# Performance work log

Measured on AMD Instinct MI355X. Metric: run time of the kernel, lower is better.

## Reference

```python
import jax, jax.numpy as jnp
import numpy as np

H = 1024      # hidden_size
V = 50257     # output_size (vocab)
L = 10        # max_length

def setup_inputs() -> dict:
    key = jax.random.key(0)
    ks = jax.random.split(key, 16)
    s = 0.02
    f = jnp.float32
    return {
        "input_idx": jax.random.randint(ks[0], (1,), 0, V),
        "hidden": jax.random.normal(ks[1], (1, 1, H), f),
        "encoder_output": jax.random.normal(ks[2], (1, H), f),      # unused by forward (as in source)
        "encoder_outputs": jax.random.normal(ks[3], (L, H), f),
        "emb": jax.random.normal(ks[4], (V, H), f) * s,
        "attn_W": jax.random.normal(ks[5], (L, 2 * H), f) * s,
        "attn_b": jnp.zeros((L,), f),
        "comb_W": jax.random.normal(ks[6], (H, 2 * H), f) * s,
        "comb_b": jnp.zeros((H,), f),
        "W_ih": jax.random.normal(ks[7], (3 * H, H), f) * s,
        "W_hh": jax.random.normal(ks[8], (3 * H, H), f) * s,
        "b_ih": jnp.zeros((3 * H,), f),
        "b_hh": jnp.zeros((3 * H,), f),
        "out_W": jax.random.normal(ks[9], (V, H), f) * s,
        "out_b": jnp.zeros((V,), f),
    }

def reference(input_idx, hidden, encoder_output, encoder_outputs,
              emb, attn_W, attn_b, comb_W, comb_b,
              W_ih, W_hh, b_ih, b_hh, out_W, out_b):
    # embedding lookup, dropout = identity (eval mode)
    embedded = emb[input_idx]                       # [1, H]
    h0 = hidden[0]                                  # [1, H]
    # additive attention over encoder outputs
    concat = jnp.concatenate([embedded, h0], axis=1)            # [1, 2H]
    attn_weights = jax.nn.softmax(concat @ attn_W.T + attn_b, axis=1)  # [1, L]
    attn_applied = attn_weights @ encoder_outputs               # [1, H]
    # combine + relu
    x = jnp.concatenate([embedded, attn_applied], axis=1) @ comb_W.T + comb_b  # [1, H]
    x = jax.nn.relu(x)
    # single GRU step (torch gate order: r, z, n)
    gi = x @ W_ih.T + b_ih                          # [1, 3H]
    gh = h0 @ W_hh.T + b_hh                         # [1, 3H]
    ir, iz, in_ = jnp.split(gi, 3, axis=1)
    hr, hz, hn = jnp.split(gh, 3, axis=1)
    r = jax.nn.sigmoid(ir + hr)
    z = jax.nn.sigmoid(iz + hz)
    n = jnp.tanh(in_ + r * hn)
    h_new = (1.0 - z) * n + z * h0                  # [1, H]
    # output projection + log-softmax
    output = jax.nn.log_softmax(h_new @ out_W.T + out_b, axis=1)  # [1, V]
    return output, h_new[None], attn_weights
```

## Files before the change

kernel.cpp:

```cpp
#include <hip/hip_runtime.h>
#include <hip/hip_bf16.h>
#include <math.h>

#define H 1024
#define V 50257
#define L 10

#define OUT_ROWS_PER_BLOCK 16
#define OUT_NBLOCKS ((V + OUT_ROWS_PER_BLOCK - 1) / OUT_ROWS_PER_BLOCK)

#define WS_CONCAT   0
#define WS_X        2048
#define WS_GH       3072
#define WS_HNEW     6144
#define WS_LOGITS   8192
#define WS_PAIRS    58880

__device__ __forceinline__ float wave_reduce(float acc) {
    #pragma unroll
    for (int off = 32; off > 0; off >>= 1) acc += __shfl_down(acc, off);
    return acc;
}

__global__ void k_attn(const int* __restrict__ idx,
                       const float* __restrict__ hidden,
                       const float* __restrict__ enc_outs,
                       const float* __restrict__ emb,
                       const float* __restrict__ attn_W,
                       const float* __restrict__ attn_b,
                       float* __restrict__ ws,
                       float* __restrict__ attnw_out) {
    __shared__ float s_w[16];
    const int t = threadIdx.x;
    const int wave = t >> 6, lane = t & 63;
    const float* erow = emb + (size_t)idx[0] * H;

    for (int i = t; i < H; i += 640) ws[WS_CONCAT + i] = erow[i];

    if (wave < L) {
        const float4* w4 = (const float4*)(attn_W + (size_t)wave * 2 * H);
        const float4* e4 = (const float4*)erow;
        const float4* h4 = (const float4*)hidden;
        float acc = 0.f;
        #pragma unroll
        for (int i = lane; i < 512; i += 64) {
            float4 a = w4[i];
            float4 x = (i < 256) ? e4[i] : h4[i - 256];
            acc += a.x * x.x + a.y * x.y + a.z * x.z + a.w * x.w;
        }
        acc = wave_reduce(acc);
        if (lane == 0) s_w[wave] = acc + attn_b[wave];
    }
    __syncthreads();
    if (t == 0) {
        float m = -1e30f;
        #pragma unroll
        for (int l = 0; l < L; ++l) m = fmaxf(m, s_w[l]);
        float s = 0.f;
        #pragma unroll
        for (int l = 0; l < L; ++l) { s_w[l] = expf(s_w[l] - m); s += s_w[l]; }
        float inv = 1.f / s;
        #pragma unroll
        for (int l = 0; l < L; ++l) s_w[l] *= inv;
    }
    __syncthreads();
    if (t < L) attnw_out[t] = s_w[t];

    for (int i = t; i < H; i += 640) {
        float acc = 0.f;
        #pragma unroll
        for (int l = 0; l < L; ++l) acc += s_w[l] * enc_outs[l * H + i];
        ws[WS_CONCAT + H + i] = acc;
    }
}

__global__ void k_comb_gh(const float* __restrict__ comb_W,
                          const float* __restrict__ comb_b,
                          const float* __restrict__ W_hh,
                          const float* __restrict__ b_hh,
                          const float* __restrict__ hidden,
                          float* __restrict__ ws) {
    const int wave = threadIdx.x >> 6, lane = threadIdx.x & 63;
    if (blockIdx.x < 256) {
        const int row = blockIdx.x * 4 + wave;
        const float4* w4 = (const float4*)(comb_W + (size_t)row * 2 * H);
        const float4* v4 = (const float4*)(ws + WS_CONCAT);
        float acc = 0.f;
        #pragma unroll
        for (int i = lane; i < 512; i += 64) {
            float4 a = w4[i], x = v4[i];
            acc += a.x * x.x + a.y * x.y + a.z * x.z + a.w * x.w;
        }
        acc = wave_reduce(acc);
        if (lane == 0) ws[WS_X + row] = fmaxf(acc + comb_b[row], 0.f);
    } else {
        const int row = (blockIdx.x - 256) * 4 + wave;
        const float4* w4 = (const float4*)(W_hh + (size_t)row * H);
        const float4* v4 = (const float4*)hidden;
        float acc = 0.f;
        #pragma unroll
        for (int i = lane; i < 256; i += 64) {
            float4 a = w4[i], x = v4[i];
            acc += a.x * x.x + a.y * x.y + a.z * x.z + a.w * x.w;
        }
        acc = wave_reduce(acc);
        if (lane == 0) ws[WS_GH + row] = acc + b_hh[row];
    }
}

__global__ void k_gi_gru(const float* __restrict__ W_ih,
                         const float* __restrict__ b_ih,
                         const float* __restrict__ hidden,
                         float* __restrict__ ws,
                         float* __restrict__ h_out) {
    const int wave = threadIdx.x >> 6, lane = threadIdx.x & 63;
    const int j = blockIdx.x * 16 + wave;
    const float4* xv = (const float4*)(ws + WS_X);
    const float4* w0 = (const float4*)(W_ih + (size_t)j * H);
    const float4* w1 = (const float4*)(W_ih + (size_t)(H + j) * H);
    const float4* w2 = (const float4*)(W_ih + (size_t)(2 * H + j) * H);
    float a0 = 0.f, a1 = 0.f, a2 = 0.f;
    #pragma unroll
    for (int i = lane; i < 256; i += 64) {
        float4 x = xv[i];
        float4 b;
        b = w0[i]; a0 += b.x * x.x + b.y * x.y + b.z * x.z + b.w * x.w;
        b = w1[i]; a1 += b.x * x.x + b.y * x.y + b.z * x.z + b.w * x.w;
        b = w2[i]; a2 += b.x * x.x + b.y * x.y + b.z * x.z + b.w * x.w;
    }
    a0 = wave_reduce(a0);
    a1 = wave_reduce(a1);
    a2 = wave_reduce(a2);
    if (lane == 0) {
        const float ir = a0 + b_ih[j];
        const float iz = a1 + b_ih[H + j];
        const float in_ = a2 + b_ih[2 * H + j];
        const float hr = ws[WS_GH + j];
        const float hz = ws[WS_GH + H + j];
        const float hn = ws[WS_GH + 2 * H + j];
        const float r = 1.f / (1.f + expf(-(ir + hr)));
        const float z = 1.f / (1.f + expf(-(iz + hz)));
        const float n = tanhf(in_ + r * hn);
        const float h0j = hidden[j];
        const float h = (1.f - z) * n + z * h0j;
        ws[WS_HNEW + j] = h;
        h_out[j] = h;
    }
}

__global__ void k_out_mv(const float* __restrict__ out_W,
                         const float* __restrict__ out_b,
                         const float* __restrict__ ws_in,
                         float* __restrict__ logits,
                         float* __restrict__ pairs) {
    __shared__ float sm[4], ss[4];
    const int wave = threadIdx.x >> 6, lane = threadIdx.x & 63;
    const int base = blockIdx.x * OUT_ROWS_PER_BLOCK + wave * 4;
    const float4* v4 = (const float4*)(ws_in + WS_HNEW);
    float vals[4];
    int nvalid = 0;
    #pragma unroll
    for (int k = 0; k < 4; ++k) {
        const int row = base + k;
        if (row >= V) break;
        const float4* w4 = (const float4*)(out_W + (size_t)row * H);
        float acc = 0.f;
        #pragma unroll
        for (int i = lane; i < 256; i += 64) {
            float4 a = w4[i], x = v4[i];
            acc += a.x * x.x + a.y * x.y + a.z * x.z + a.w * x.w;
        }
        acc = wave_reduce(acc);
        if (lane == 0) {
            const float val = acc + out_b[row];
            logits[row] = val;
            vals[nvalid] = val;
        }
        ++nvalid;
    }
    if (lane == 0) {
        float m = -INFINITY, s = 0.f;
        for (int k = 0; k < nvalid; ++k) m = fmaxf(m, vals[k]);
        for (int k = 0; k < nvalid; ++k) s += expf(vals[k] - m);
        sm[wave] = m; ss[wave] = s;
    }
    __syncthreads();
    if (threadIdx.x == 0) {
        float m = -INFINITY, s = 0.f;
        #pragma unroll
        for (int w = 0; w < 4; ++w) {
            const float pm = sm[w], psv = ss[w];
            if (pm == -INFINITY) continue;
            if (m == -INFINITY) { m = pm; s = psv; }
            else if (pm <= m)   { s += psv * expf(pm - m); }
            else                { s = s * expf(m - pm) + psv; m = pm; }
        }
        pairs[2 * blockIdx.x]     = m;
        pairs[2 * blockIdx.x + 1] = s;
    }
}

__global__ void k_write(const float* __restrict__ logits,
                        const float* __restrict__ pairs,
                        float* __restrict__ out) {
    __shared__ float sm[256], ss[256];
    const int t = threadIdx.x;
    float m = -INFINITY, s = 0.f;
    for (int i = t; i < OUT_NBLOCKS; i += 256) {
        const float pm = pairs[2 * i], psv = pairs[2 * i + 1];
        if (pm == -INFINITY) continue;
        if (m == -INFINITY) { m = pm; s = psv; }
        else if (pm <= m)   { s += psv * expf(pm - m); }
        else                { s = s * expf(m - pm) + psv; m = pm; }
    }
    sm[t] = m; ss[t] = s; __syncthreads();
    for (int k = 128; k > 0; k >>= 1) {
        if (t < k) {
            const float pm = sm[t + k], psv = ss[t + k];
            float cm = sm[t], cs = ss[t];
            if (pm != -INFINITY) {
                if (cm == -INFINITY) { cm = pm; cs = psv; }
                else if (pm <= cm)   { cs += psv * expf(pm - cm); }
                else                 { cs = cs * expf(cm - pm) + psv; cm = pm; }
            }
            sm[t] = cm; ss[t] = cs;
        }
        __syncthreads();
    }
    const float M = sm[0];
    const float LS = logf(ss[0]);
    const int i = blockIdx.x * 256 + t;
    if (i < V) out[i] = logits[i] - M - LS;
}

extern "C" void kernel_launch(void* const* d_in, const int* in_sizes, int n_in,
                              void* d_out, int out_size, void* d_ws, size_t ws_size,
                              hipStream_t stream) {
    const int*   idx      = (const int*)  d_in[0];
    const float* hidden   = (const float*)d_in[1];
    const float* enc_outs = (const float*)d_in[3];
    const float* emb      = (const float*)d_in[4];
    const float* attn_W   = (const float*)d_in[5];
    const float* attn_b   = (const float*)d_in[6];
    const float* comb_W   = (const float*)d_in[7];
    const float* comb_b   = (const float*)d_in[8];
    const float* W_ih     = (const float*)d_in[9];
    const float* W_hh     = (const float*)d_in[10];
    const float* b_ih     = (const float*)d_in[11];
    const float* b_hh     = (const float*)d_in[12];
    const float* out_W    = (const float*)d_in[13];
    const float* out_b    = (const float*)d_in[14];

    float* ws  = (float*)d_ws;
    float* out = (float*)d_out;

    k_attn<<<1, 640, 0, stream>>>(idx, hidden, enc_outs, emb, attn_W, attn_b,
                                  ws, out + V + H);
    k_comb_gh<<<1024, 256, 0, stream>>>(comb_W, comb_b, W_hh, b_hh, hidden, ws);
    k_gi_gru<<<64, 1024, 0, stream>>>(W_ih, b_ih, hidden, ws, out + V);
    k_out_mv<<<OUT_NBLOCKS, 256, 0, stream>>>(out_W, out_b, ws,
                                              ws + WS_LOGITS, ws + WS_PAIRS);
    k_write<<<(V + 255) / 256, 256, 0, stream>>>(ws + WS_LOGITS, ws + WS_PAIRS, out);
}
```

Measured before the change: 60.82 us.

## Fold attention into combine via precomputed encoder projections, merging first two kernels

Removes the serial single-block attention kernel by computing comb_W's second half against each encoder output (10 columns) in parallel with the attention softmax, W_hh gate projection and embedding half of comb. The GRU kernel then reconstructs x as half1 + sum_l aw_l * M2T[l] before its matvec, so one launch and one dependency stage are removed. This trades extra FLOPs (10 dot products per comb row) and more workspace traffic for fewer serialized stages. Vectors are also hoisted into registers in the matvec loops.

```diff
diff --git a/kernel.cpp b/kernel.cpp
--- a/kernel.cpp
+++ b/kernel.cpp
@@ -6,134 +6,169 @@
 #define V 50257
 #define L 10
 
-#define OUT_ROWS_PER_BLOCK 16
-#define OUT_NBLOCKS ((V + OUT_ROWS_PER_BLOCK - 1) / OUT_ROWS_PER_BLOCK)
-
-#define WS_CONCAT   0
-#define WS_X        2048
-#define WS_GH       3072
-#define WS_HNEW     6144
-#define WS_LOGITS   8192
-#define WS_PAIRS    58880
-
-__device__ __forceinline__ float wave_reduce(float acc) {
-    #pragma unroll
-    for (int off = 32; off > 0; off >>= 1) acc += __shfl_down(acc, off);
-    return acc;
-}
-
-__global__ void k_attn(const int* __restrict__ idx,
-                       const float* __restrict__ hidden,
-                       const float* __restrict__ enc_outs,
-                       const float* __restrict__ emb,
-                       const float* __restrict__ attn_W,
-                       const float* __restrict__ attn_b,
-                       float* __restrict__ ws,
-                       float* __restrict__ attnw_out) {
-    __shared__ float s_w[16];
-    const int t = threadIdx.x;
+#define RPC 16
+#define NCHUNK ((V + RPC - 1) / RPC)
+
+#define WS_AW     0
+#define WS_GH     16
+#define WS_HALF1  3104
+#define WS_M2T    4128
+#define WS_HNEW   14368
+#define WS_LOGITS 15392
+#define WS_PAIRS  65664
+
+__device__ __forceinline__ float wave_reduce(float a) {
+    #pragma unroll
+    for (int off = 32; off > 0; off >>= 1) a += __shfl_down(a, off);
+    return a;
+}
+
+__device__ __forceinline__ void lse_merge(float& m, float& s, float pm, float ps) {
+    if (pm == -INFINITY) return;
+    if (m == -INFINITY)  { m = pm; s = ps; }
+    else if (pm <= m)    { s += ps * expf(pm - m); }
+    else                 { s = s * expf(m - pm) + ps; m = pm; }
+}
+
+__device__ __forceinline__ float dot4(float4 a, float4 x) {
+    return a.x * x.x + a.y * x.y + a.z * x.z + a.w * x.w;
+}
+
+__global__ __launch_bounds__(256) void k_stage1(
+    const int* __restrict__ idx, const float* __restrict__ hidden,
+    const float* __restrict__ enc_outs, const float* __restrict__ emb,
+    const float* __restrict__ attn_W, const float* __restrict__ attn_b,
+    const float* __restrict__ W_hh, const float* __restrict__ b_hh,
+    const float* __restrict__ comb_W,
+    float* __restrict__ ws, float* __restrict__ aw_out)
+{
+    const int b = blockIdx.x, t = threadIdx.x;
     const int wave = t >> 6, lane = t & 63;
     const float* erow = emb + (size_t)idx[0] * H;
 
-    for (int i = t; i < H; i += 640) ws[WS_CONCAT + i] = erow[i];
-
-    if (wave < L) {
-        const float4* w4 = (const float4*)(attn_W + (size_t)wave * 2 * H);
+    if (b == 0) {
+        __shared__ float s_w[16];
         const float4* e4 = (const float4*)erow;
         const float4* h4 = (const float4*)hidden;
-        float acc = 0.f;
-        #pragma unroll
-        for (int i = lane; i < 512; i += 64) {
-            float4 a = w4[i];
-            float4 x = (i < 256) ? e4[i] : h4[i - 256];
-            acc += a.x * x.x + a.y * x.y + a.z * x.z + a.w * x.w;
-        }
-        acc = wave_reduce(acc);
-        if (lane == 0) s_w[wave] = acc + attn_b[wave];
+        for (int l = wave; l < L; l += 4) {
+            const float4* w4 = (const float4*)(attn_W + (size_t)l * 2 * H);
+            float acc = 0.f;
+            #pragma unroll
+            for (int ii = 0; ii < 8; ++ii) {
+                const int i = lane + 64 * ii;
+                const float4 a = w4[i];
+                const float4 x = (i < 256) ? e4[i] : h4[i - 256];
+                acc += dot4(a, x);
+            }
+            acc = wave_reduce(acc);
+            if (lane == 0) s_w[l] = acc + attn_b[l];
+        }
+        __syncthreads();
+        if (t == 0) {
+            float m = -1e30f;
+            #pragma unroll
+            for (int l = 0; l < L; ++l) m = fmaxf(m, s_w[l]);
+            float s = 0.f;
+            #pragma unroll
+            for (int l = 0; l < L; ++l) { s_w[l] = expf(s_w[l] - m); s += s_w[l]; }
+            const float inv = 1.f / s;
+            #pragma unroll
+            for (int l = 0; l < L; ++l) s_w[l] *= inv;
+        }
+        __syncthreads();
+        if (t < L) { ws[WS_AW + t] = s_w[t]; aw_out[t] = s_w[t]; }
+    } else if (b <= 192) {
+        const int r0 = (b - 1) * 16 + wave * 4;
+        const float4* v4 = (const float4*)hidden;
+        float4 hx[4];
+        #pragma unroll
+        for (int j = 0; j < 4; ++j) hx[j] = v4[lane + 64 * j];
+        #pragma unroll
+        for (int k = 0; k < 4; ++k) {
+            const int row = r0 + k;
+            const float4* w4 = (const float4*)(W_hh + (size_t)row * H);
+            float acc = 0.f;
+            #pragma unroll
+            for (int j = 0; j < 4; ++j) acc += dot4(w4[lane + 64 * j], hx[j]);
+            acc = wave_reduce(acc);
+            if (lane == 0) ws[WS_GH + row] = acc + b_hh[row];
+        }
+    } else if (b <= 256) {
+        const int r0 = (b - 193) * 16 + wave * 4;
+        const float4* e4 = (const float4*)erow;
+        float4 ex[4];
+        #pragma unroll
+        for (int j = 0; j < 4; ++j) ex[j] = e4[lane + 64 * j];
+        #pragma unroll
+        for (int k = 0; k < 4; ++k) {
+            const int row = r0 + k;
+            const float4* w4 = (const float4*)(comb_W + (size_t)row * 2 * H);
+            float acc = 0.f;
+            #pragma unroll
+            for (int j = 0; j < 4; ++j) acc += dot4(w4[lane + 64 * j], ex[j]);
+            acc = wave_reduce(acc);
+            if (lane == 0) ws[WS_HALF1 + row] = acc;
+        }
+    } else {
+        const int r = (b - 257) * 4 + wave;
+        const float4* w4 = (const float4*)(comb_W + (size_t)r * 2 * H + H);
+        float acc[L];
+        #pragma unroll
+        for (int l = 0; l < L; ++l) acc[l] = 0.f;
+        #pragma unroll
+        for (int j = 0; j < 4; ++j) {
+            const int i = lane + 64 * j;
+            const float4 w = w4[i];
+            #pragma unroll
+            for (int l = 0; l < L; ++l) {
+                const float4 e = ((const float4*)(enc_outs + l * H))[i];
+                acc[l] += dot4(w, e);
+            }
+        }
+        #pragma unroll
+        for (int l = 0; l < L; ++l) {
+            const float r_ = wave_reduce(acc[l]);
+            if (lane == 0) ws[WS_M2T + l * 1024 + r] = r_;
+        }
+    }
+}
+
+__global__ __launch_bounds__(1024) void k_gi_gru(
+    const float* __restrict__ W_ih, const float* __restrict__ b_ih,
+    const float* __restrict__ comb_b, const float* __restrict__ hidden,
+    float* __restrict__ ws, float* __restrict__ h_out)
+{
+    __shared__ float sx[1024];
+    const int t = threadIdx.x;
+    {
+        float acc = ws[WS_HALF1 + t] + comb_b[t];
+        #pragma unroll
+        for (int l = 0; l < L; ++l)
+            acc += ws[WS_M2T + l * 1024 + t] * ws[WS_AW + l];
+        sx[t] = fmaxf(acc, 0.f);
     }
     __syncthreads();
-    if (t == 0) {
-        float m = -1e30f;
-        #pragma unroll
-        for (int l = 0; l < L; ++l) m = fmaxf(m, s_w[l]);
-        float s = 0.f;
-        #pragma unroll
-        for (int l = 0; l < L; ++l) { s_w[l] = expf(s_w[l] - m); s += s_w[l]; }
-        float inv = 1.f / s;
-        #pragma unroll
-        for (int l = 0; l < L; ++l) s_w[l] *= inv;
-    }
-    __syncthreads();
-    if (t < L) attnw_out[t] = s_w[t];
-
-    for (int i = t; i < H; i += 640) {
-        float acc = 0.f;
-        #pragma unroll
-        for (int l = 0; l < L; ++l) acc += s_w[l] * enc_outs[l * H + i];
-        ws[WS_CONCAT + H + i] = acc;
-    }
-}
-
-__global__ void k_comb_gh(const float* __restrict__ comb_W,
-                          const float* __restrict__ comb_b,
-                          const float* __restrict__ W_hh,
-                          const float* __restrict__ b_hh,
-                          const float* __restrict__ hidden,
-                          float* __restrict__ ws) {
-    const int wave = threadIdx.x >> 6, lane = threadIdx.x & 63;
-    if (blockIdx.x < 256) {
-        const int row = blockIdx.x * 4 + wave;
-        const float4* w4 = (const float4*)(comb_W + (size_t)row * 2 * H);
-        const float4* v4 = (const float4*)(ws + WS_CONCAT);
-        float acc = 0.f;
-        #pragma unroll
-        for (int i = lane; i < 512; i += 64) {
-            float4 a = w4[i], x = v4[i];
-            acc += a.x * x.x + a.y * x.y + a.z * x.z + a.w * x.w;
-        }
-        acc = wave_reduce(acc);
-        if (lane == 0) ws[WS_X + row] = fmaxf(acc + comb_b[row], 0.f);
-    } else {
-        const int row = (blockIdx.x - 256) * 4 + wave;
-        const float4* w4 = (const float4*)(W_hh + (size_t)row * H);
-        const float4* v4 = (const float4*)hidden;
-        float acc = 0.f;
-        #pragma unroll
-        for (int i = lane; i < 256; i += 64) {
-            float4 a = w4[i], x = v4[i];
-            acc += a.x * x.x + a.y * x.y + a.z * x.z + a.w * x.w;
-        }
-        acc = wave_reduce(acc);
-        if (lane == 0) ws[WS_GH + row] = acc + b_hh[row];
-    }
-}
-
-__global__ void k_gi_gru(const float* __restrict__ W_ih,
-                         const float* __restrict__ b_ih,
-                         const float* __restrict__ hidden,
-                         float* __restrict__ ws,
-                         float* __restrict__ h_out) {
-    const int wave = threadIdx.x >> 6, lane = threadIdx.x & 63;
+    const int wave = t >> 6, lane = t & 63;
     const int j = blockIdx.x * 16 + wave;
-    const float4* xv = (const float4*)(ws + WS_X);
+    const float4* x4 = (const float4*)sx;
+    float4 xx[4];
+    #pragma unroll
+    for (int q = 0; q < 4; ++q) xx[q] = x4[lane + 64 * q];
     const float4* w0 = (const float4*)(W_ih + (size_t)j * H);
     const float4* w1 = (const float4*)(W_ih + (size_t)(H + j) * H);
     const float4* w2 = (const float4*)(W_ih + (size_t)(2 * H + j) * H);
     float a0 = 0.f, a1 = 0.f, a2 = 0.f;
     #pragma unroll
-    for (int i = lane; i < 256; i += 64) {
-        float4 x = xv[i];
-        float4 b;
-        b = w0[i]; a0 += b.x * x.x + b.y * x.y + b.z * x.z + b.w * x.w;
-        b = w1[i]; a1 += b.x * x.x + b.y * x.y + b.z * x.z + b.w * x.w;
-        b = w2[i]; a2 += b.x * x.x + b.y * x.y + b.z * x.z + b.w * x.w;
-    }
-    a0 = wave_reduce(a0);
-    a1 = wave_reduce(a1);
-    a2 = wave_reduce(a2);
+    for (int q = 0; q < 4; ++q) {
+        const int i = lane + 64 * q;
+        a0 += dot4(w0[i], xx[q]);
+        a1 += dot4(w1[i], xx[q]);
+        a2 += dot4(w2[i], xx[q]);
+    }
+    a0 = wave_reduce(a0); a1 = wave_reduce(a1); a2 = wave_reduce(a2);
     if (lane == 0) {
-        const float ir = a0 + b_ih[j];
-        const float iz = a1 + b_ih[H + j];
+        const float ir  = a0 + b_ih[j];
+        const float iz  = a1 + b_ih[H + j];
         const float in_ = a2 + b_ih[2 * H + j];
         const float hr = ws[WS_GH + j];
         const float hz = ws[WS_GH + H + j];
@@ -141,94 +176,69 @@
         const float r = 1.f / (1.f + expf(-(ir + hr)));
         const float z = 1.f / (1.f + expf(-(iz + hz)));
         const float n = tanhf(in_ + r * hn);
-        const float h0j = hidden[j];
-        const float h = (1.f - z) * n + z * h0j;
+        const float h = (1.f - z) * n + z * hidden[j];
         ws[WS_HNEW + j] = h;
         h_out[j] = h;
     }
 }
 
-__global__ void k_out_mv(const float* __restrict__ out_W,
-                         const float* __restrict__ out_b,
-                         const float* __restrict__ ws_in,
-                         float* __restrict__ logits,
-                         float* __restrict__ pairs) {
+__global__ __launch_bounds__(256) void k_out_mv(
+    const float* __restrict__ out_W, const float* __restrict__ out_b,
+    const float* __restrict__ ws_in, float* __restrict__ logits,
+    float* __restrict__ pairs)
+{
     __shared__ float sm[4], ss[4];
     const int wave = threadIdx.x >> 6, lane = threadIdx.x & 63;
-    const int base = blockIdx.x * OUT_ROWS_PER_BLOCK + wave * 4;
+    const int base = blockIdx.x * RPC + wave * 4;
     const float4* v4 = (const float4*)(ws_in + WS_HNEW);
-    float vals[4];
-    int nvalid = 0;
+    float4 hx[4];
+    #pragma unroll
+    for (int j = 0; j < 4; ++j) hx[j] = v4[lane + 64 * j];
+    float wm = -INFINITY, wsum = 0.f;
     #pragma unroll
     for (int k = 0; k < 4; ++k) {
         const int row = base + k;
-        if (row >= V) break;
-        const float4* w4 = (const float4*)(out_W + (size_t)row * H);
-        float acc = 0.f;
-        #pragma unroll
-        for (int i = lane; i < 256; i += 64) {
-            float4 a = w4[i], x = v4[i];
-            acc += a.x * x.x + a.y * x.y + a.z * x.z + a.w * x.w;
-        }
-        acc = wave_reduce(acc);
-        if (lane == 0) {
-            const float val = acc + out_b[row];
-            logits[row] = val;
-            vals[nvalid] = val;
-        }
-        ++nvalid;
-    }
-    if (lane == 0) {
-        float m = -INFINITY, s = 0.f;
-        for (int k = 0; k < nvalid; ++k) m = fmaxf(m, vals[k]);
-        for (int k = 0; k < nvalid; ++k) s += expf(vals[k] - m);
-        sm[wave] = m; ss[wave] = s;
-    }
+        if (row < V) {
+            const float4* w4 = (const float4*)(out_W + (size_t)row * H);
+            float acc = 0.f;
+            #pragma unroll
+            for (int j = 0; j < 4; ++j) acc += dot4(w4[lane + 64 * j], hx[j]);
+            acc = wave_reduce(acc);
+            if (lane == 0) {
+                const float val = acc + out_b[row];
+                logits[row] = val;
+                lse_merge(wm, wsum, val, 1.f);
+            }
+        }
+    }
+    if (lane == 0) { sm[wave] = wm; ss[wave] = wsum; }
     __syncthreads();
     if (threadIdx.x == 0) {
         float m = -INFINITY, s = 0.f;
         #pragma unroll
-        for (int w = 0; w < 4; ++w) {
-            const float pm = sm[w], psv = ss[w];
-            if (pm == -INFINITY) continue;
-            if (m == -INFINITY) { m = pm; s = psv; }
-            else if (pm <= m)   { s += psv * expf(pm - m); }
-            else                { s = s * expf(m - pm) + psv; m = pm; }
-        }
-        pairs[2 * blockIdx.x]     = m;
-        pairs[2 * blockIdx.x + 1] = s;
-    }
-}
-
-__global__ void k_write(const float* __restrict__ logits,
-                        const float* __restrict__ pairs,
-                        float* __restrict__ out) {
+        for (int w = 0; w < 4; ++w) lse_merge(m, s, sm[w], ss[w]);
+        pairs[2 * blockIdx.x] = m; pairs[2 * blockIdx.x + 1] = s;
+    }
+}
+
+__global__ __launch_bounds__(256) void k_write(
+    const float* __restrict__ logits, const float* __restrict__ pairs,
+    float* __restrict__ out)
+{
     __shared__ float sm[256], ss[256];
     const int t = threadIdx.x;
     float m = -INFINITY, s = 0.f;
-    for (int i = t; i < OUT_NBLOCKS; i += 256) {
-        const float pm = pairs[2 * i], psv = pairs[2 * i + 1];
-        if (pm == -INFINITY) continue;
-        if (m == -INFINITY) { m = pm; s = psv; }
-        else if (pm <= m)   { s += psv * expf(pm - m); }
-        else                { s = s * expf(m - pm) + psv; m = pm; }
-    }
+    for (int i = t; i < NCHUNK; i += 256) lse_merge(m, s, pairs[2 * i], pairs[2 * i + 1]);
     sm[t] = m; ss[t] = s; __syncthreads();
     for (int k = 128; k > 0; k >>= 1) {
         if (t < k) {
-            const float pm = sm[t + k], psv = ss[t + k];
-            float cm = sm[t], cs = ss[t];
-            if (pm != -INFINITY) {
-                if (cm == -INFINITY) { cm = pm; cs = psv; }
-                else if (pm <= cm)   { cs += psv * expf(pm - cm); }
-                else                 { cs = cs * expf(cm - pm) + psv; cm = pm; }
-            }
-            sm[t] = cm; ss[t] = cs;
+            float mm = sm[t], ssv = ss[t];
+            lse_merge(mm, ssv, sm[t + k], ss[t + k]);
+            sm[t] = mm; ss[t] = ssv;
         }
         __syncthreads();
     }
-    const float M = sm[0];
-    const float LS = logf(ss[0]);
+    const float M = sm[0], LS = logf(ss[0]);
     const int i = blockIdx.x * 256 + t;
     if (i < V) out[i] = logits[i] - M - LS;
 }
@@ -254,11 +264,11 @@
     float* ws  = (float*)d_ws;
     float* out = (float*)d_out;
 
-    k_attn<<<1, 640, 0, stream>>>(idx, hidden, enc_outs, emb, attn_W, attn_b,
-                                  ws, out + V + H);
-    k_comb_gh<<<1024, 256, 0, stream>>>(comb_W, comb_b, W_hh, b_hh, hidden, ws);
-    k_gi_gru<<<64, 1024, 0, stream>>>(W_ih, b_ih, hidden, ws, out + V);
-    k_out_mv<<<OUT_NBLOCKS, 256, 0, stream>>>(out_W, out_b, ws,
-                                              ws + WS_LOGITS, ws + WS_PAIRS);
+    k_stage1<<<513, 256, 0, stream>>>(idx, hidden, enc_outs, emb,
+                                      attn_W, attn_b, W_hh, b_hh, comb_W,
+                                      ws, out + V + H);
+    k_gi_gru<<<64, 1024, 0, stream>>>(W_ih, b_ih, comb_b, hidden, ws, out + V);
+    k_out_mv<<<NCHUNK, 256, 0, stream>>>(out_W, out_b, ws,
+                                         ws + WS_LOGITS, ws + WS_PAIRS);
     k_write<<<(V + 255) / 256, 256, 0, stream>>>(ws + WS_LOGITS, ws + WS_PAIRS, out);
 }
```

New measurement: 59.50 us. 2.2% less time.
